# Kernel tuning notes

Hardware: AMD Instinct MI355X
Metric: run time of the kernel (lower is better)

Reference implementation:

```python
import jax, jax.numpy as jnp
import numpy as np

HIDDEN = 3072
HEADS = 24
HEAD_DIM = HIDDEN // HEADS  # 128
MLP_HIDDEN = 4 * HIDDEN     # 12288
IMG_LEN = 1024
TXT_LEN = 256
L = IMG_LEN + TXT_LEN
B = 1
EPS = 1e-6


def setup_inputs() -> dict:
    key = jax.random.key(0)
    ks = jax.random.split(key, 12)
    x = jax.random.normal(ks[0], (B, L, HIDDEN), jnp.float32)
    vec = jax.random.normal(ks[1], (B, HIDDEN), jnp.float32)
    # RoPE tables: real cos/sin of position * inv_freq, repeated over pairs (full head_dim)
    inv_freq = 1.0 / (10000.0 ** (np.arange(0, HEAD_DIM, 2, dtype=np.float32) / HEAD_DIM))
    theta = np.arange(IMG_LEN, dtype=np.float32)[:, None] * inv_freq[None, :]  # [img_len, D/2]
    theta = np.repeat(theta, 2, axis=-1)  # [img_len, D]
    freqs_cos = jnp.asarray(np.cos(theta))[None, :, None, :]  # [1, img_len, 1, D]
    freqs_sin = jnp.asarray(np.sin(theta))[None, :, None, :]
    s = 0.02
    mod_w = jax.random.normal(ks[2], (HIDDEN, 3 * HIDDEN), jnp.float32) * s
    mod_b = jnp.zeros((3 * HIDDEN,), jnp.float32)
    w1 = jax.random.normal(ks[3], (HIDDEN, 3 * HIDDEN + MLP_HIDDEN), jnp.float32) * s
    b1 = jnp.zeros((3 * HIDDEN + MLP_HIDDEN,), jnp.float32)
    w2 = jax.random.normal(ks[4], (HIDDEN + MLP_HIDDEN, HIDDEN), jnp.float32) * s
    b2 = jnp.zeros((HIDDEN,), jnp.float32)
    qn_w = jnp.ones((HEAD_DIM,), jnp.float32)
    kn_w = jnp.ones((HEAD_DIM,), jnp.float32)
    cu_seqlens_q = jnp.array([0, IMG_LEN, L], jnp.int32)
    cu_seqlens_kv = jnp.array([0, IMG_LEN, L], jnp.int32)
    return {"x": x, "vec": vec, "freqs_cos": freqs_cos, "freqs_sin": freqs_sin,
            "mod_w": mod_w, "mod_b": mod_b, "w1": w1, "b1": b1, "w2": w2, "b2": b2,
            "qn_w": qn_w, "kn_w": kn_w, "img_len": IMG_LEN,
            "cu_seqlens_q": cu_seqlens_q, "cu_seqlens_kv": cu_seqlens_kv}


def _layernorm(x):  # elementwise_affine=False
    mu = jnp.mean(x, axis=-1, keepdims=True)
    var = jnp.mean(jnp.square(x - mu), axis=-1, keepdims=True)
    return (x - mu) * jax.lax.rsqrt(var + EPS)


def _rmsnorm(x, w):
    ms = jnp.mean(jnp.square(x), axis=-1, keepdims=True)
    return x * jax.lax.rsqrt(ms + EPS) * w


def _rope_interleaved(x, cos, sin):
    # mode=1: rotate interleaved pairs: (-x1, x0, -x3, x2, ...)
    x0 = x[..., 0::2]
    x1 = x[..., 1::2]
    rot = jnp.stack([-x1, x0], axis=-1).reshape(x.shape)
    return x * cos + rot * sin


def reference(x, vec, freqs_cos, freqs_sin, mod_w, mod_b, w1, b1, w2, b2,
              qn_w, kn_w, img_len, cu_seqlens_q, cu_seqlens_kv):
    bs = x.shape[0]
    assert cu_seqlens_q.shape[0] == 2 * bs + 1
    # adaLN modulation: SiLU -> Linear(hidden, 3*hidden)
    mod = jax.nn.silu(vec) @ mod_w + mod_b           # [B, 3H]
    mod = mod[:, None, :]                             # [B, 1, 3H]
    mod_shift, mod_scale, mod_gate = jnp.split(mod, 3, axis=-1)
    x_mod = _layernorm(x) * (1.0 + mod_scale) + mod_shift
    # fused QKV + MLP projection
    h = x_mod @ w1 + b1                               # [B, L, 3*hidden + mlp]
    qkv = h[..., :3 * HIDDEN]
    mlp = h[..., 3 * HIDDEN:]
    # 'B L (K H D) -> K B L H D'
    qkv = qkv.reshape(bs, -1, 3, HEADS, HEAD_DIM)
    q, k, v = qkv[:, :, 0], qkv[:, :, 1], qkv[:, :, 2]  # [B, L, H, D]
    q = _rmsnorm(q, qn_w)
    k = _rmsnorm(k, kn_w)
    # RoPE on image tokens only
    img_q = _rope_interleaved(q[:, :img_len], freqs_cos, freqs_sin)
    img_k = _rope_interleaved(k[:, :img_len], freqs_cos, freqs_sin)
    q = jnp.concatenate([img_q, q[:, img_len:]], axis=1)
    k = jnp.concatenate([img_k, k[:, img_len:]], axis=1)
    # dense attention (bs==1 path, no mask), scale = 1/sqrt(head_dim)
    scale = 1.0 / jnp.sqrt(jnp.float32(HEAD_DIM))
    scores = jnp.einsum('bqhd,bkhd->bhqk', q, k) * scale
    probs = jax.nn.softmax(scores, axis=-1)
    attn = jnp.einsum('bhqk,bkhd->bqhd', probs, v)
    attn = attn.reshape(bs, -1, HEADS * HEAD_DIM)     # [B, L, hidden]
    # output projection on concat(attn, gelu_tanh(mlp))
    out = jnp.concatenate([attn, jax.nn.gelu(mlp, approximate=True)], axis=-1) @ w2 + b2
    return x + out * mod_gate
```

## Files before the change

### kernel.cpp

```cpp
#include <hip/hip_runtime.h>
#include <cstdint>
#include <cstddef>

typedef __bf16 bf16x8_t __attribute__((ext_vector_type(8)));
typedef float f32x4 __attribute__((ext_vector_type(4)));

#define HID 3072
#define NHEADS 24
#define HD 128
#define MLP 12288
#define SEQ 1280
#define IMG 1024
#define N1 21504
#define QKVW 9216
#define A2W 15360
#define EPSV 1e-6f

__device__ __forceinline__ size_t tpos(int row, int col, int KT) {
    return ((size_t)(row >> 8) * KT + (col >> 6)) * 16384
         + (size_t)(((((col >> 5) & 1) << 4) + ((row >> 4) & 15)) * 512
                    + (((row & 15) + (((col >> 3) & 3) << 4)) << 3) + (col & 7));
}

__device__ __forceinline__ void gload16(const void* g, void* l) {
    __builtin_amdgcn_global_load_lds(
        (const __attribute__((address_space(1))) unsigned int*)g,
        (__attribute__((address_space(3))) unsigned int*)l, 16, 0, 0);
}

__device__ __forceinline__ void bar() {
    asm volatile("" ::: "memory");
    __builtin_amdgcn_s_barrier();
    asm volatile("" ::: "memory");
}

__global__ void silu_kernel(const float* __restrict__ v, float* __restrict__ sv) {
    int i = blockIdx.x * 256 + threadIdx.x;
    float x = v[i];
    sv[i] = x / (1.f + expf(-x));
}

__global__ void gemv_part(const float* __restrict__ sv, const float* __restrict__ W,
                          float* __restrict__ part) {
    int n = blockIdx.x * 256 + threadIdx.x;
    int k0 = blockIdx.y * 384;
    float s = 0.f;
    for (int k = k0; k < k0 + 384; ++k)
        s = fmaf(sv[k], W[(size_t)k * QKVW + n], s);
    part[(size_t)blockIdx.y * QKVW + n] = s;
}

__global__ void gemv_reduce(const float* __restrict__ part, const float* __restrict__ bias,
                            float* __restrict__ mod) {
    int n = blockIdx.x * 256 + threadIdx.x;
    float s = bias[n];
    #pragma unroll
    for (int ky = 0; ky < 8; ++ky) s += part[(size_t)ky * QKVW + n];
    mod[n] = s;
}

__global__ __launch_bounds__(384) void ln_mod_kernel(const float* __restrict__ x,
                                                     const float* __restrict__ mod,
                                                     ushort* __restrict__ xmt) {
    int m = blockIdx.x;
    int t = threadIdx.x;
    int lane = t & 63, w = t >> 6;
    const float* xr = x + (size_t)m * HID;
    float4 v0 = *reinterpret_cast<const float4*>(&xr[t * 8]);
    float4 v1 = *reinterpret_cast<const float4*>(&xr[t * 8 + 4]);
    float s = v0.x + v0.y + v0.z + v0.w + v1.x + v1.y + v1.z + v1.w;
    float sq = v0.x * v0.x + v0.y * v0.y + v0.z * v0.z + v0.w * v0.w +
               v1.x * v1.x + v1.y * v1.y + v1.z * v1.z + v1.w * v1.w;
    #pragma unroll
    for (int off = 1; off < 64; off <<= 1) {
        s += __shfl_xor(s, off);
        sq += __shfl_xor(sq, off);
    }
    __shared__ float red[12];
    if (lane == 0) { red[w] = s; red[w + 6] = sq; }
    __syncthreads();
    s = red[0] + red[1] + red[2] + red[3] + red[4] + red[5];
    sq = red[6] + red[7] + red[8] + red[9] + red[10] + red[11];
    float mu = s * (1.f / HID);
    float var = sq * (1.f / HID) - mu * mu;
    float rs = rsqrtf(var + EPSV);
    float vals[8] = {v0.x, v0.y, v0.z, v0.w, v1.x, v1.y, v1.z, v1.w};
    union { ushort u[8]; uint4 q; } pk;
    #pragma unroll
    for (int j = 0; j < 8; ++j) {
        int n = t * 8 + j;
        float y = (vals[j] - mu) * rs * (1.f + mod[HID + n]) + mod[n];
        pk.u[j] = __builtin_bit_cast(ushort, (__bf16)y);
    }
    *reinterpret_cast<uint4*>(&xmt[tpos(m, t * 8, HID >> 6)]) = pk.q;
}

__global__ __launch_bounds__(256) void convB_kernel(const float* __restrict__ in,
                                                    ushort* __restrict__ out, int K, int N) {
    __shared__ float tle[64][65];
    int KT = K >> 6;
    int kb = blockIdx.x % KT, nb = blockIdx.x / KT;
    int k0 = kb * 64, n0 = nb * 64;
    int tid = threadIdx.x;
    int rr = tid >> 2, cg = (tid & 3) * 16;
    #pragma unroll
    for (int j = 0; j < 4; ++j) {
        float4 vv = *reinterpret_cast<const float4*>(&in[(size_t)(k0 + rr) * N + n0 + cg + j * 4]);
        tle[rr][cg + j * 4 + 0] = vv.x;
        tle[rr][cg + j * 4 + 1] = vv.y;
        tle[rr][cg + j * 4 + 2] = vv.z;
        tle[rr][cg + j * 4 + 3] = vv.w;
    }
    __syncthreads();
    int nl = tid & 63;
    #pragma unroll
    for (int gg = 0; gg < 2; ++gg) {
        int g = (tid >> 6) + gg * 4;
        union { ushort u[8]; uint4 q; } pk;
        #pragma unroll
        for (int j = 0; j < 8; ++j)
            pk.u[j] = __builtin_bit_cast(ushort, (__bf16)tle[g * 8 + j][nl]);
        *reinterpret_cast<uint4*>(&out[tpos(n0 + nl, k0 + g * 8, KT)]) = pk.q;
    }
}

template <int EPI, int SPLITS>
__global__ __launch_bounds__(512, 2) void gemm8p(
    const ushort* __restrict__ At, const ushort* __restrict__ Bt,
    const float* __restrict__ bias, float* __restrict__ outf, ushort* __restrict__ outb,
    int KTtot, int NTloc, int NTN) {
    int nwg = gridDim.x;
    int q = nwg >> 3, r = nwg & 7;
    int orig = blockIdx.x;
    int xcd = orig & 7;
    int wgid = (xcd < r ? xcd * (q + 1) : r * (q + 1) + (xcd - r) * q) + (orig >> 3);
    int mt = wgid % 5;
    int p = wgid / 5;
    int nt = p % NTN;
    int sp = p / NTN;
    int kOff = sp * NTloc;
    int m0 = mt * 256, n0 = nt * 256;

    __shared__ ushort LA[2][16384];
    __shared__ ushort LB[2][16384];

    int tid = threadIdx.x;
    int lane = tid & 63, wid = tid >> 6;
    int wm = wid >> 2, wn = wid & 3;
    int lr = lane & 15, lg = lane >> 4;

    const ushort* gA = At + (size_t)mt * KTtot * 16384;
    const ushort* gB = Bt + (size_t)nt * KTtot * 16384;

    f32x4 acc[8][4] = {};
    bf16x8_t af0[4][2], af1[4][2], bf0[2][2], bf1[2][2];

    auto stage = [&](ushort (*L)[16384], int buf, const ushort* g, int ktG) {
        #pragma unroll
        for (int j = 0; j < 4; ++j) {
            int b = wid * 4 + j;
            gload16(g + (size_t)ktG * 16384 + b * 512 + lane * 8, &L[buf][b * 512]);
        }
    };
    auto rdA = [&](int buf, int h, bf16x8_t (&af)[4][2]) {
        #pragma unroll
        for (int mi = 0; mi < 4; ++mi)
            #pragma unroll
            for (int k = 0; k < 2; ++k)
                af[mi][k] = *reinterpret_cast<const bf16x8_t*>(
                    &LA[buf][(k * 16 + wm * 8 + h * 4 + mi) * 512 + lane * 8]);
    };
    auto rdB = [&](int buf, int v, bf16x8_t (&bf)[2][2]) {
        #pragma unroll
        for (int ni = 0; ni < 2; ++ni)
            #pragma unroll
            for (int k = 0; k < 2; ++k)
                bf[ni][k] = *reinterpret_cast<const bf16x8_t*>(
                    &LB[buf][(k * 16 + wn * 4 + v * 2 + ni) * 512 + lane * 8]);
    };
    auto mmq = [&](bf16x8_t (&af)[4][2], bf16x8_t (&bf)[2][2], int h, int v) {
        __builtin_amdgcn_s_setprio(1);
        #pragma unroll
        for (int mi = 0; mi < 4; ++mi)
            #pragma unroll
            for (int ni = 0; ni < 2; ++ni)
                #pragma unroll
                for (int k = 0; k < 2; ++k)
                    acc[h * 4 + mi][v * 2 + ni] = __builtin_amdgcn_mfma_f32_16x16x32_bf16(
                        af[mi][k], bf[ni][k], acc[h * 4 + mi][v * 2 + ni], 0, 0, 0);
        __builtin_amdgcn_s_setprio(0);
    };

    stage(LA, 0, gA, kOff);
    stage(LB, 0, gB, kOff);
    stage(LA, 1, gA, kOff + 1);
    stage(LB, 1, gB, kOff + 1);
    asm volatile("s_waitcnt vmcnt(8)" ::: "memory");
    bar();
    rdA(0, 0, af0);
    rdB(0, 0, bf0);

    for (int t = 0; t < NTloc; ++t) {
        int c = t & 1;
        rdB(c, 1, bf1);
        mmq(af0, bf0, 0, 0);
        bar();
        rdA(c, 1, af1);
        mmq(af0, bf1, 0, 1);
        bar();
        if (t + 2 < NTloc) stage(LA, c, gA, kOff + t + 2);
        mmq(af1, bf0, 1, 0);
        if (t + 1 < NTloc) {
            if (t + 2 < NTloc) asm volatile("s_waitcnt vmcnt(4)" ::: "memory");
            else               asm volatile("s_waitcnt vmcnt(0)" ::: "memory");
        }
        bar();
        if (t + 1 < NTloc) {
            rdA(c ^ 1, 0, af0);
            rdB(c ^ 1, 0, bf0);
        }
        if (t + 2 < NTloc) stage(LB, c, gB, kOff + t + 2);
        mmq(af1, bf1, 1, 1);
        bar();
    }

    #pragma unroll
    for (int mi8 = 0; mi8 < 8; ++mi8) {
        #pragma unroll
        for (int nj = 0; nj < 4; ++nj) {
            int col = n0 + wn * 64 + nj * 16 + lr;
            #pragma unroll
            for (int rr2 = 0; rr2 < 4; ++rr2) {
                int row = m0 + wm * 128 + mi8 * 16 + lg * 4 + rr2;
                float val = acc[mi8][nj][rr2];
                if (EPI == 1) {
                    val += bias[col];
                    if (n0 < QKVW) {
                        outf[(size_t)row * QKVW + col] = val;
                    } else {
                        float u = 0.7978845608028654f * (val + 0.044715f * val * val * val);
                        float g = val / (1.f + __expf(-2.f * u));
                        outb[tpos(row, HID + (col - QKVW), A2W >> 6)] =
                            __builtin_bit_cast(ushort, (__bf16)g);
                    }
                } else {
                    outf[(size_t)(sp * SEQ + row) * HID + col] = val;
                }
            }
        }
    }
}

__global__ __launch_bounds__(256) void ksplit_reduce(const float* __restrict__ part,
                                                     const float* __restrict__ x,
                                                     const float* __restrict__ bias,
                                                     const float* __restrict__ gate,
                                                     float* __restrict__ out) {
    int i = blockIdx.x * 256 + threadIdx.x;
    int col = (i % (HID / 4)) * 4;
    f32x4 a = *reinterpret_cast<const f32x4*>(&part[(size_t)i * 4]);
    #pragma unroll
    for (int s = 1; s < 4; ++s) {
        f32x4 p = *reinterpret_cast<const f32x4*>(&part[(size_t)s * SEQ * HID + (size_t)i * 4]);
        #pragma unroll
        for (int c = 0; c < 4; ++c) a[c] += p[c];
    }
    f32x4 xv = *reinterpret_cast<const f32x4*>(&x[(size_t)i * 4]);
    f32x4 bv = *reinterpret_cast<const f32x4*>(&bias[col]);
    f32x4 gv = *reinterpret_cast<const f32x4*>(&gate[col]);
    f32x4 o;
    #pragma unroll
    for (int c = 0; c < 4; ++c) o[c] = xv[c] + (a[c] + bv[c]) * gv[c];
    *reinterpret_cast<f32x4*>(&out[(size_t)i * 4]) = o;
}

__global__ __launch_bounds__(256) void qkv_post(const float* __restrict__ h,
                                                const float* __restrict__ fc,
                                                const float* __restrict__ fs,
                                                const float* __restrict__ qn,
                                                const float* __restrict__ kn,
                                                __bf16* __restrict__ qb,
                                                __bf16* __restrict__ kb,
                                                __bf16* __restrict__ vb) {
    int m = blockIdx.x;
    int lane = threadIdx.x & 63, w = threadIdx.x >> 6;
    for (int rr = w; rr < 72; rr += 4) {
        int s = rr / 24, hd = rr % 24;
        const float* src = h + (size_t)m * QKVW + s * HID + hd * HD;
        float2 xv = *reinterpret_cast<const float2*>(&src[2 * lane]);
        float x0 = xv.x, x1 = xv.y;
        if (s < 2) {
            float ss = x0 * x0 + x1 * x1;
            #pragma unroll
            for (int off = 1; off < 64; off <<= 1) ss += __shfl_xor(ss, off);
            float rs = rsqrtf(ss * (1.f / HD) + EPSV);
            const float* nw = (s == 0) ? qn : kn;
            x0 *= rs * nw[2 * lane];
            x1 *= rs * nw[2 * lane + 1];
            if (m < IMG) {
                float c0 = fc[m * HD + 2 * lane], c1 = fc[m * HD + 2 * lane + 1];
                float s0 = fs[m * HD + 2 * lane], s1 = fs[m * HD + 2 * lane + 1];
                float r0 = x0 * c0 - x1 * s0;
                float r1 = x1 * c1 + x0 * s1;
                x0 = r0; x1 = r1;
            }
        }
        __bf16* dst = ((s == 0) ? qb : (s == 1) ? kb : vb) + (size_t)hd * SEQ * HD + (size_t)m * HD + 2 * lane;
        ushort u0 = __builtin_bit_cast(ushort, (__bf16)x0);
        ushort u1 = __builtin_bit_cast(ushort, (__bf16)x1);
        *reinterpret_cast<uint*>(dst) = (uint)u0 | ((uint)u1 << 16);
    }
}

__global__ __launch_bounds__(256) void attn_kernel(const __bf16* __restrict__ qb,
                                                   const __bf16* __restrict__ kb,
                                                   const __bf16* __restrict__ vb,
                                                   ushort* __restrict__ a2) {
    int head = blockIdx.y;
    int tid = threadIdx.x;
    int lane = tid & 63, w = tid >> 6;
    int lr = lane & 15, lg = lane >> 4;
    int q0 = blockIdx.x * 64 + w * 16;
    const __bf16* Q = qb + (size_t)head * SEQ * HD;
    const __bf16* Kp = kb + (size_t)head * SEQ * HD;
    const __bf16* Vp = vb + (size_t)head * SEQ * HD;

    bf16x8_t qf[4];
    #pragma unroll
    for (int kc = 0; kc < 4; ++kc)
        qf[kc] = *reinterpret_cast<const bf16x8_t*>(&Q[(size_t)(q0 + lr) * HD + kc * 32 + lg * 8]);

    __shared__ alignas(16) __bf16 Kl[32][136];
    __shared__ alignas(16) __bf16 Vl[32][136];
    __shared__ float Pl[4][32][16];

    float m_run = -1e30f, l_run = 0.f;
    f32x4 of[8] = {};
    const float sm_scale = 0.08838834764831845f;

    for (int kv0 = 0; kv0 < SEQ; kv0 += 32) {
        #pragma unroll
        for (int cc = 0; cc < 2; ++cc) {
            int c = tid + cc * 256;
            int row = c >> 4, off = (c & 15) * 8;
            *reinterpret_cast<bf16x8_t*>(&Kl[row][off]) =
                *reinterpret_cast<const bf16x8_t*>(&Kp[(size_t)(kv0 + row) * HD + off]);
            *reinterpret_cast<bf16x8_t*>(&Vl[row][off]) =
                *reinterpret_cast<const bf16x8_t*>(&Vp[(size_t)(kv0 + row) * HD + off]);
        }
        __syncthreads();

        f32x4 st[2] = {};
        #pragma unroll
        for (int h = 0; h < 2; ++h)
            #pragma unroll
            for (int kc = 0; kc < 4; ++kc) {
                bf16x8_t kf = *reinterpret_cast<const bf16x8_t*>(&Kl[h * 16 + lr][kc * 32 + lg * 8]);
                st[h] = __builtin_amdgcn_mfma_f32_16x16x32_bf16(kf, qf[kc], st[h], 0, 0, 0);
            }
        float sarr[8];
        #pragma unroll
        for (int h = 0; h < 2; ++h)
            #pragma unroll
            for (int r = 0; r < 4; ++r) sarr[h * 4 + r] = st[h][r] * sm_scale;

        float mloc = sarr[0];
        #pragma unroll
        for (int i = 1; i < 8; ++i) mloc = fmaxf(mloc, sarr[i]);
        mloc = fmaxf(mloc, __shfl_xor(mloc, 16));
        mloc = fmaxf(mloc, __shfl_xor(mloc, 32));
        float m_new = fmaxf(m_run, mloc);
        float alpha = expf(m_run - m_new);
        float pv[8], psum = 0.f;
        #pragma unroll
        for (int i = 0; i < 8; ++i) { pv[i] = expf(sarr[i] - m_new); psum += pv[i]; }
        psum += __shfl_xor(psum, 16);
        psum += __shfl_xor(psum, 32);
        l_run = l_run * alpha + psum;
        m_run = m_new;

        #pragma unroll
        for (int h = 0; h < 2; ++h)
            #pragma unroll
            for (int r = 0; r < 4; ++r) Pl[w][h * 16 + lg * 4 + r][lr] = pv[h * 4 + r];
        bf16x8_t pa;
        #pragma unroll
        for (int j = 0; j < 8; ++j) pa[j] = (__bf16)Pl[w][lg * 8 + j][lr];

        float alr[4];
        #pragma unroll
        for (int r = 0; r < 4; ++r) alr[r] = __shfl(alpha, lg * 4 + r);

        #pragma unroll
        for (int db = 0; db < 8; ++db) {
            #pragma unroll
            for (int r = 0; r < 4; ++r) of[db][r] *= alr[r];
            bf16x8_t vv;
            #pragma unroll
            for (int j = 0; j < 8; ++j) vv[j] = Vl[lg * 8 + j][db * 16 + lr];
            of[db] = __builtin_amdgcn_mfma_f32_16x16x32_bf16(pa, vv, of[db], 0, 0, 0);
        }
        __syncthreads();
    }

    float lr4[4];
    #pragma unroll
    for (int r = 0; r < 4; ++r) lr4[r] = __shfl(l_run, lg * 4 + r);
    #pragma unroll
    for (int db = 0; db < 8; ++db)
        #pragma unroll
        for (int r = 0; r < 4; ++r) {
            int row = q0 + lg * 4 + r;
            int col = head * HD + db * 16 + lr;
            a2[tpos(row, col, A2W >> 6)] =
                __builtin_bit_cast(ushort, (__bf16)(of[db][r] / lr4[r]));
        }
}

extern "C" void kernel_launch(void* const* d_in, const int* in_sizes, int n_in,
                              void* d_out, int out_size, void* d_ws, size_t ws_size,
                              hipStream_t stream) {
    const float* x = (const float*)d_in[0];
    const float* vec = (const float*)d_in[1];
    const float* fc = (const float*)d_in[2];
    const float* fs = (const float*)d_in[3];
    const float* mod_w = (const float*)d_in[4];
    const float* mod_b = (const float*)d_in[5];
    const float* w1 = (const float*)d_in[6];
    const float* b1 = (const float*)d_in[7];
    const float* w2 = (const float*)d_in[8];
    const float* b2 = (const float*)d_in[9];
    const float* qn = (const float*)d_in[10];
    const float* kn = (const float*)d_in[11];
    float* out = (float*)d_out;

    char* ws = (char*)d_ws;
    size_t off = 0;
    float* sv = (float*)(ws + off); off += 3072 * 4;
    float* mod = (float*)(ws + off); off += 9216 * 4;
    float* part = (float*)(ws + off); off += 8 * 9216 * 4;
    off = (off + 255) & ~(size_t)255;
    ushort* xmt = (ushort*)(ws + off); off += (size_t)SEQ * HID * 2;
    off = (off + 255) & ~(size_t)255;
    float* hqkv = (float*)(ws + off); off += (size_t)SEQ * QKVW * 4;
    __bf16* qb = (__bf16*)(ws + off); off += (size_t)NHEADS * SEQ * HD * 2;
    __bf16* kb = (__bf16*)(ws + off); off += (size_t)NHEADS * SEQ * HD * 2;
    __bf16* vb = (__bf16*)(ws + off); off += (size_t)NHEADS * SEQ * HD * 2;
    off = (off + 255) & ~(size_t)255;
    ushort* a2t = (ushort*)(ws + off); off += (size_t)SEQ * A2W * 2;
    float* part2 = hqkv;

    off = (off + 255) & ~(size_t)255;
    ushort* w1b = (ushort*)(ws + off);
    ushort* w2b = w1b;

    silu_kernel<<<12, 256, 0, stream>>>(vec, sv);
    gemv_part<<<dim3(36, 8), 256, 0, stream>>>(sv, mod_w, part);
    gemv_reduce<<<36, 256, 0, stream>>>(part, mod_b, mod);
    ln_mod_kernel<<<SEQ, 384, 0, stream>>>(x, mod, xmt);

    convB_kernel<<<(HID / 64) * (N1 / 64), 256, 0, stream>>>(w1, w1b, HID, N1);
    gemm8p<1, 1><<<5 * (N1 / 256), 512, 0, stream>>>(xmt, w1b, b1, hqkv, a2t,
                                                     HID / 64, HID / 64, N1 / 256);
    convB_kernel<<<(A2W / 64) * (HID / 64), 256, 0, stream>>>(w2, w2b, A2W, HID);
    qkv_post<<<SEQ, 256, 0, stream>>>(hqkv, fc, fs, qn, kn, qb, kb, vb);
    attn_kernel<<<dim3(SEQ / 64, NHEADS), 256, 0, stream>>>(qb, kb, vb, a2t);
    gemm8p<2, 4><<<4 * 5 * (HID / 256), 512, 0, stream>>>(a2t, w2b, nullptr, part2, nullptr,
                                                          A2W / 64, A2W / 64 / 4, HID / 256);
    ksplit_reduce<<<SEQ * HID / 1024, 256, 0, stream>>>(part2, x, b2, mod + 2 * HID, out);
}
```

Measured before the change: 653.7 us.

## Fold weight bf16 conversions into gemv and attention kernels as extra blocks

The separate w1 and w2 fp32-to-bf16 tiled conversion kernels are merged into other launches. The w1 conversion runs as extra blocks inside the modulation gemv kernel, and the w2 conversion runs as extra blocks inside the attention kernel. This removes two launches and lets the bandwidth-bound conversion overlap with latency-bound gemv and compute-bound attention. The cost is that attention blocks now carry extra shared memory for the conversion tile, which may lower attention occupancy, and block scheduling order between the two workloads is not controlled.

```diff
diff --git a/kernel.cpp b/kernel.cpp
--- a/kernel.cpp
+++ b/kernel.cpp
@@ -34,20 +34,57 @@
     asm volatile("" ::: "memory");
 }
 
+__device__ __forceinline__ void conv_tile(const float* __restrict__ in, ushort* __restrict__ out,
+                                          int N, int KT, int kb, int nb, int tid,
+                                          float (*tle)[65]) {
+    int k0 = kb * 64, n0 = nb * 64;
+    int rr = tid >> 2, cg = (tid & 3) * 16;
+    #pragma unroll
+    for (int j = 0; j < 4; ++j) {
+        float4 vv = *reinterpret_cast<const float4*>(&in[(size_t)(k0 + rr) * N + n0 + cg + j * 4]);
+        tle[rr][cg + j * 4 + 0] = vv.x;
+        tle[rr][cg + j * 4 + 1] = vv.y;
+        tle[rr][cg + j * 4 + 2] = vv.z;
+        tle[rr][cg + j * 4 + 3] = vv.w;
+    }
+    __syncthreads();
+    int nl = tid & 63;
+    #pragma unroll
+    for (int gg = 0; gg < 2; ++gg) {
+        int g = (tid >> 6) + gg * 4;
+        union { ushort u[8]; uint4 q; } pk;
+        #pragma unroll
+        for (int j = 0; j < 8; ++j)
+            pk.u[j] = __builtin_bit_cast(ushort, (__bf16)tle[g * 8 + j][nl]);
+        *reinterpret_cast<uint4*>(&out[tpos(n0 + nl, k0 + g * 8, KT)]) = pk.q;
+    }
+}
+
 __global__ void silu_kernel(const float* __restrict__ v, float* __restrict__ sv) {
     int i = blockIdx.x * 256 + threadIdx.x;
     float x = v[i];
     sv[i] = x / (1.f + expf(-x));
 }
 
-__global__ void gemv_part(const float* __restrict__ sv, const float* __restrict__ W,
-                          float* __restrict__ part) {
-    int n = blockIdx.x * 256 + threadIdx.x;
-    int k0 = blockIdx.y * 384;
-    float s = 0.f;
-    for (int k = k0; k < k0 + 384; ++k)
-        s = fmaf(sv[k], W[(size_t)k * QKVW + n], s);
-    part[(size_t)blockIdx.y * QKVW + n] = s;
+__global__ __launch_bounds__(256) void gemvconv_fat(const float* __restrict__ sv,
+                                                    const float* __restrict__ W,
+                                                    float* __restrict__ part,
+                                                    const float* __restrict__ w1,
+                                                    ushort* __restrict__ w1b) {
+    __shared__ float tle[64][65];
+    int bid = blockIdx.x;
+    int tid = threadIdx.x;
+    if (bid < 288) {
+        int n = (bid % 36) * 256 + tid;
+        int k0 = (bid / 36) * 384;
+        float s = 0.f;
+        for (int k = k0; k < k0 + 384; ++k)
+            s = fmaf(sv[k], W[(size_t)k * QKVW + n], s);
+        part[(size_t)(bid / 36) * QKVW + n] = s;
+        return;
+    }
+    int cb = bid - 288;
+    conv_tile(w1, w1b, N1, HID / 64, cb % 48, cb / 48, tid, tle);
 }
 
 __global__ void gemv_reduce(const float* __restrict__ part, const float* __restrict__ bias,
@@ -93,35 +130,6 @@
         pk.u[j] = __builtin_bit_cast(ushort, (__bf16)y);
     }
     *reinterpret_cast<uint4*>(&xmt[tpos(m, t * 8, HID >> 6)]) = pk.q;
-}
-
-__global__ __launch_bounds__(256) void convB_kernel(const float* __restrict__ in,
-                                                    ushort* __restrict__ out, int K, int N) {
-    __shared__ float tle[64][65];
-    int KT = K >> 6;
-    int kb = blockIdx.x % KT, nb = blockIdx.x / KT;
-    int k0 = kb * 64, n0 = nb * 64;
-    int tid = threadIdx.x;
-    int rr = tid >> 2, cg = (tid & 3) * 16;
-    #pragma unroll
-    for (int j = 0; j < 4; ++j) {
-        float4 vv = *reinterpret_cast<const float4*>(&in[(size_t)(k0 + rr) * N + n0 + cg + j * 4]);
-        tle[rr][cg + j * 4 + 0] = vv.x;
-        tle[rr][cg + j * 4 + 1] = vv.y;
-        tle[rr][cg + j * 4 + 2] = vv.z;
-        tle[rr][cg + j * 4 + 3] = vv.w;
-    }
-    __syncthreads();
-    int nl = tid & 63;
-    #pragma unroll
-    for (int gg = 0; gg < 2; ++gg) {
-        int g = (tid >> 6) + gg * 4;
-        union { ushort u[8]; uint4 q; } pk;
-        #pragma unroll
-        for (int j = 0; j < 8; ++j)
-            pk.u[j] = __builtin_bit_cast(ushort, (__bf16)tle[g * 8 + j][nl]);
-        *reinterpret_cast<uint4*>(&out[tpos(n0 + nl, k0 + g * 8, KT)]) = pk.q;
-    }
 }
 
 template <int EPI, int SPLITS>
@@ -312,15 +320,28 @@
     }
 }
 
-__global__ __launch_bounds__(256) void attn_kernel(const __bf16* __restrict__ qb,
-                                                   const __bf16* __restrict__ kb,
-                                                   const __bf16* __restrict__ vb,
-                                                   ushort* __restrict__ a2) {
-    int head = blockIdx.y;
+__global__ __launch_bounds__(256) void attn_fat(const __bf16* __restrict__ qb,
+                                                const __bf16* __restrict__ kb,
+                                                const __bf16* __restrict__ vb,
+                                                ushort* __restrict__ a2,
+                                                const float* __restrict__ w2,
+                                                ushort* __restrict__ w2b) {
+    __shared__ float tle[64][65];
+    int bid = blockIdx.x;
     int tid = threadIdx.x;
+    if (bid >= 480) {
+        int cb = bid - 480;
+        conv_tile(w2, w2b, HID, A2W / 64, cb % 240, cb / 240, tid, tle);
+        return;
+    }
+    __shared__ alignas(16) __bf16 Kl[32][136];
+    __shared__ alignas(16) __bf16 Vl[32][136];
+    __shared__ float Pl[4][32][16];
+
+    int head = bid / 20;
     int lane = tid & 63, w = tid >> 6;
     int lr = lane & 15, lg = lane >> 4;
-    int q0 = blockIdx.x * 64 + w * 16;
+    int q0 = (bid % 20) * 64 + w * 16;
     const __bf16* Q = qb + (size_t)head * SEQ * HD;
     const __bf16* Kp = kb + (size_t)head * SEQ * HD;
     const __bf16* Vp = vb + (size_t)head * SEQ * HD;
@@ -329,10 +350,6 @@
     #pragma unroll
     for (int kc = 0; kc < 4; ++kc)
         qf[kc] = *reinterpret_cast<const bf16x8_t*>(&Q[(size_t)(q0 + lr) * HD + kc * 32 + lg * 8]);
-
-    __shared__ alignas(16) __bf16 Kl[32][136];
-    __shared__ alignas(16) __bf16 Vl[32][136];
-    __shared__ float Pl[4][32][16];
 
     float m_run = -1e30f, l_run = 0.f;
     f32x4 of[8] = {};
@@ -455,16 +472,14 @@
     ushort* w2b = w1b;
 
     silu_kernel<<<12, 256, 0, stream>>>(vec, sv);
-    gemv_part<<<dim3(36, 8), 256, 0, stream>>>(sv, mod_w, part);
+    gemvconv_fat<<<288 + 48 * 336, 256, 0, stream>>>(sv, mod_w, part, w1, w1b);
     gemv_reduce<<<36, 256, 0, stream>>>(part, mod_b, mod);
     ln_mod_kernel<<<SEQ, 384, 0, stream>>>(x, mod, xmt);
 
-    convB_kernel<<<(HID / 64) * (N1 / 64), 256, 0, stream>>>(w1, w1b, HID, N1);
     gemm8p<1, 1><<<5 * (N1 / 256), 512, 0, stream>>>(xmt, w1b, b1, hqkv, a2t,
                                                      HID / 64, HID / 64, N1 / 256);
-    convB_kernel<<<(A2W / 64) * (HID / 64), 256, 0, stream>>>(w2, w2b, A2W, HID);
     qkv_post<<<SEQ, 256, 0, stream>>>(hqkv, fc, fs, qn, kn, qb, kb, vb);
-    attn_kernel<<<dim3(SEQ / 64, NHEADS), 256, 0, stream>>>(qb, kb, vb, a2t);
+    attn_fat<<<480 + 240 * 48, 256, 0, stream>>>(qb, kb, vb, a2t, w2, w2b);
     gemm8p<2, 4><<<4 * 5 * (HID / 256), 512, 0, stream>>>(a2t, w2b, nullptr, part2, nullptr,
                                                           A2W / 64, A2W / 64 / 4, HID / 256);
     ksplit_reduce<<<SEQ * HID / 1024, 256, 0, stream>>>(part2, x, b2, mod + 2 * HID, out);
```

New measurement: 628.1 us. 3.9% less time.
